# Kernel optimization log

Hardware: AMD Instinct MI355X
Metric: run time of the kernel (lower is better)

The kernel has to match this reference:

```python
import jax, jax.numpy as jnp
import numpy as np

B, S, E = 4, 2048, 1024
H, HD, R = 16, 64, 32  # heads, head_dim, rank


def setup_inputs() -> dict:
    key = jax.random.key(0)
    ks = jax.random.split(key, 9)
    sc = 0.02
    return {
        "hidden_states": jax.random.normal(ks[0], (B, S, E), jnp.float32),
        "q_weight": jax.random.normal(ks[1], (E, E), jnp.float32) * sc,
        "q_bias": jax.random.normal(ks[2], (E,), jnp.float32) * sc,
        "k_weight": jax.random.normal(ks[3], (E, E), jnp.float32) * sc,
        "k_bias": jax.random.normal(ks[4], (E,), jnp.float32) * sc,
        "low_rank_value_weight": jax.random.normal(ks[5], (E, H * R), jnp.float32) * sc,
        "low_rank_value_bias": jax.random.normal(ks[6], (H * R,), jnp.float32) * sc,
        "low_rank_output_weight": jax.random.normal(ks[7], (H * R, E), jnp.float32) * sc,
        "output_bias": jax.random.normal(ks[8], (E,), jnp.float32) * sc,
    }


def reference(hidden_states, q_weight, q_bias, k_weight, k_bias,
              low_rank_value_weight, low_rank_value_bias,
              low_rank_output_weight, output_bias):
    b, s, _ = hidden_states.shape
    q = hidden_states @ q_weight + q_bias                       # [B,S,E]
    k = hidden_states @ k_weight + k_bias                       # [B,S,E]
    v = hidden_states @ low_rank_value_weight + low_rank_value_bias  # [B,S,H*R]
    q = q.reshape(b, s, H, HD).transpose(0, 2, 1, 3)            # [B,H,S,HD]
    k = k.reshape(b, s, H, HD).transpose(0, 2, 1, 3)
    v = v.reshape(b, s, H, R).transpose(0, 2, 1, 3)             # [B,H,S,R]
    scores = jnp.einsum('bhqd,bhkd->bhqk', q, k) / jnp.sqrt(jnp.float32(HD))
    causal = jnp.tril(jnp.ones((s, s), dtype=bool))
    scores = jnp.where(causal, scores, jnp.finfo(scores.dtype).min)
    probs = jax.nn.softmax(scores, axis=-1)                     # [B,H,S,S]
    attn = jnp.einsum('bhqk,bhkr->bhqr', probs, v)              # [B,H,S,R]
    attn = attn.transpose(0, 2, 1, 3).reshape(b, s, H * R)      # [B,S,H*R]
    out = attn @ low_rank_output_weight + output_bias           # [B,S,E]
    return out
```

## Files before the change

kernel.cpp:

```cpp
#include <hip/hip_runtime.h>

typedef _Float16 f16;
typedef __attribute__((ext_vector_type(4))) float f4;
typedef __attribute__((ext_vector_type(4))) _Float16 h4;
typedef __attribute__((ext_vector_type(8))) _Float16 h8;
typedef __attribute__((ext_vector_type(4))) float f32x4;
typedef __attribute__((ext_vector_type(4))) unsigned int u4;

#define SWZ(row, colByte) (((row) << 7) + ((colByte) ^ (((row) & 7) << 4)))

__global__ __launch_bounds__(256) void cast_f16(
    const float* __restrict__ in, f16* __restrict__ out, int n4) {
  for (int i = blockIdx.x * 256 + threadIdx.x; i < n4; i += gridDim.x * 256) {
    const f4 v = ((const f4*)in)[i];
    h4 h;
    h.x = (f16)v.x; h.y = (f16)v.y; h.z = (f16)v.z; h.w = (f16)v.w;
    ((h4*)out)[i] = h;
  }
}

__global__ __launch_bounds__(256) void transpose_cast(
    const float* __restrict__ in, f16* __restrict__ out, int R, int C) {
  __shared__ float tile[32][33];
  const int t = threadIdx.x, tx = t & 31, ty = t >> 5;
  const int bc = blockIdx.x * 32, br = blockIdx.y * 32;
#pragma unroll
  for (int i = 0; i < 4; ++i)
    tile[ty + i * 8][tx] = in[(size_t)(br + ty + i * 8) * C + bc + tx];
  __syncthreads();
#pragma unroll
  for (int i = 0; i < 4; ++i)
    out[(size_t)(bc + ty + i * 8) * R + br + tx] = (f16)tile[tx][ty + i * 8];
}

__global__ __launch_bounds__(256) void hgemm_qkv(
    const f16* __restrict__ A, const f16* __restrict__ Bt,
    const float* __restrict__ qb, const float* __restrict__ kb,
    const float* __restrict__ vb,
    f16* __restrict__ qf, f16* __restrict__ kf, f16* __restrict__ vf) {
  __shared__ f16 As[128 * 40];
  __shared__ f16 Bs[128 * 40];
  const int K = 1024;
  const int id = blockIdx.x;
  const int swz = (id & 7) * 160 + (id >> 3);
  const int bnT = swz % 20;
  const int bm = (swz / 20) * 128;
  const int bn = bnT * 128;
  const int t = threadIdx.x;
  const int lane = t & 63, wave = t >> 6;
  const int wr = wave >> 1, wc = wave & 1;
  const int lrow = lane & 15, lk = lane >> 4;

  f32x4 acc[4][4];
#pragma unroll
  for (int i = 0; i < 4; ++i)
#pragma unroll
    for (int j = 0; j < 4; ++j) acc[i][j] = (f32x4)0.f;

  for (int kt = 0; kt < K; kt += 32) {
#pragma unroll
    for (int i = 0; i < 2; ++i) {
      const int ch = t + i * 256;
      const int row = ch >> 2, part = ch & 3;
      *(u4*)&As[row * 40 + part * 8] =
          *(const u4*)(A + (size_t)(bm + row) * K + kt + part * 8);
      *(u4*)&Bs[row * 40 + part * 8] =
          *(const u4*)(Bt + (size_t)(bn + row) * K + kt + part * 8);
    }
    __syncthreads();
    h8 af[4], bf[4];
#pragma unroll
    for (int f = 0; f < 4; ++f) {
      af[f] = *(const h8*)&As[(wr * 64 + f * 16 + lrow) * 40 + lk * 8];
      bf[f] = *(const h8*)&Bs[(wc * 64 + f * 16 + lrow) * 40 + lk * 8];
    }
#pragma unroll
    for (int i = 0; i < 4; ++i)
#pragma unroll
      for (int j = 0; j < 4; ++j)
        acc[i][j] = __builtin_amdgcn_mfma_f32_16x16x32_f16(af[i], bf[j], acc[i][j], 0, 0, 0);
    __syncthreads();
  }

  const float* bias;
  f16* outp;
  int nbase;
  if (bnT < 8) { bias = qb; outp = qf; nbase = 0; }
  else if (bnT < 16) { bias = kb; outp = kf; nbase = 1024; }
  else { bias = vb; outp = vf; nbase = 2048; }

#pragma unroll
  for (int fi = 0; fi < 4; ++fi) {
#pragma unroll
    for (int j = 0; j < 4; ++j) {
      const int grow = bm + wr * 64 + fi * 16 + lk * 4 + j;
      const int bb = grow >> 11, ss = grow & 2047;
#pragma unroll
      for (int fj = 0; fj < 4; ++fj) {
        const int gcol = bn + wc * 64 + fj * 16 + lrow;
        const int nl = gcol - nbase;
        const float g = acc[fi][fj][j] + bias[nl];
        if (bnT < 16) {
          outp[((size_t)(bb * 16 + (nl >> 6)) * 2048 + ss) * 64 + (nl & 63)] = (f16)g;
        } else {
          outp[((size_t)(bb * 16 + (nl >> 5)) * 2048 + ss) * 32 + (nl & 31)] = (f16)g;
        }
      }
    }
  }
}

__global__ __launch_bounds__(256) void hgemm_out(
    const f16* __restrict__ A, const f16* __restrict__ Bt,
    const float* __restrict__ bias, float* __restrict__ outp,
    const int N, const int K) {
  __shared__ f16 As[128 * 40];
  __shared__ f16 Bs[128 * 40];
  const int id = blockIdx.x;
  const int swz = (id & 7) * 64 + (id >> 3);
  const int bn = (swz & 7) * 128;
  const int bm = (swz >> 3) * 128;
  const int t = threadIdx.x;
  const int lane = t & 63, wave = t >> 6;
  const int wr = wave >> 1, wc = wave & 1;
  const int lrow = lane & 15, lk = lane >> 4;

  f32x4 acc[4][4];
#pragma unroll
  for (int i = 0; i < 4; ++i)
#pragma unroll
    for (int j = 0; j < 4; ++j) acc[i][j] = (f32x4)0.f;

  for (int kt = 0; kt < K; kt += 32) {
#pragma unroll
    for (int i = 0; i < 2; ++i) {
      const int ch = t + i * 256;
      const int row = ch >> 2, part = ch & 3;
      *(u4*)&As[row * 40 + part * 8] =
          *(const u4*)(A + (size_t)(bm + row) * K + kt + part * 8);
      *(u4*)&Bs[row * 40 + part * 8] =
          *(const u4*)(Bt + (size_t)(bn + row) * K + kt + part * 8);
    }
    __syncthreads();
    h8 af[4], bf[4];
#pragma unroll
    for (int f = 0; f < 4; ++f) {
      af[f] = *(const h8*)&As[(wr * 64 + f * 16 + lrow) * 40 + lk * 8];
      bf[f] = *(const h8*)&Bs[(wc * 64 + f * 16 + lrow) * 40 + lk * 8];
    }
#pragma unroll
    for (int i = 0; i < 4; ++i)
#pragma unroll
      for (int j = 0; j < 4; ++j)
        acc[i][j] = __builtin_amdgcn_mfma_f32_16x16x32_f16(af[i], bf[j], acc[i][j], 0, 0, 0);
    __syncthreads();
  }

#pragma unroll
  for (int fi = 0; fi < 4; ++fi) {
#pragma unroll
    for (int j = 0; j < 4; ++j) {
      const int grow = bm + wr * 64 + fi * 16 + lk * 4 + j;
#pragma unroll
      for (int fj = 0; fj < 4; ++fj) {
        const int gcol = bn + wc * 64 + fj * 16 + lrow;
        outp[(size_t)grow * N + gcol] = acc[fi][fj][j] + bias[gcol];
      }
    }
  }
}

__global__ __launch_bounds__(256) void attn_mfma(
    const f16* __restrict__ qf, const f16* __restrict__ kf,
    const f16* __restrict__ vf, f16* __restrict__ attf) {
  __shared__ f16 Ks[64 * 64];
  __shared__ f16 VsT[32 * 64];
  __shared__ f16 Ps[4 * 32 * 64];
  const int id = blockIdx.x;
  const int bh = id & 63;
  const int qblk = 15 - (id >> 6);
  const int qbase = qblk * 128;
  const int t = threadIdx.x;
  const int lane = t & 63, w = t >> 6;
  const int l15 = lane & 15, g = lane >> 4;
  const size_t kvbase = (size_t)bh * 2048;
  char* Pw = (char*)&Ps[w * 32 * 64];

  h8 qreg[2][2];
#pragma unroll
  for (int fj = 0; fj < 2; ++fj) {
    const int q = qbase + fj * 64 + w * 16 + l15;
#pragma unroll
    for (int ks = 0; ks < 2; ++ks) {
      h8 raw = *(const h8*)(qf + (kvbase + q) * 64 + ks * 32 + g * 8);
#pragma unroll
      for (int e = 0; e < 8; ++e) raw[e] = raw[e] * (f16)0.125f;
      qreg[fj][ks] = raw;
    }
  }

  f32x4 accO[2][2];
#pragma unroll
  for (int i = 0; i < 2; ++i)
#pragma unroll
    for (int j = 0; j < 2; ++j) accO[i][j] = (f32x4)0.f;
  float m2[2] = {-1.0e30f, -1.0e30f};
  float lsum[2] = {0.f, 0.f};

  const int ntiles = qblk * 2 + 2;
  for (int kt = 0; kt < ntiles; ++kt) {
    const int kbase = kt * 64;
    __syncthreads();
#pragma unroll
    for (int i = 0; i < 2; ++i) {
      const int idx = t + i * 256;
      const int row = idx >> 3, ch = idx & 7;
      *(u4*)((char*)Ks + SWZ(row, ch * 16)) =
          *(const u4*)(kf + (kvbase + kbase + row) * 64 + ch * 8);
    }
    {
      const int key = t >> 2, ch = t & 3;
      const u4 wv = *(const u4*)(vf + (kvbase + kbase + key) * 32 + ch * 8);
      const h8 hv = __builtin_bit_cast(h8, wv);
#pragma unroll
      for (int e = 0; e < 8; ++e) {
        const int row = ch * 8 + e;
        *(f16*)((char*)VsT + SWZ(row, key * 2)) = hv[e];
      }
    }
    __syncthreads();

    f32x4 accS[4][2];
#pragma unroll
    for (int i = 0; i < 4; ++i)
#pragma unroll
      for (int j = 0; j < 2; ++j) accS[i][j] = (f32x4)0.f;
#pragma unroll
    for (int ks = 0; ks < 2; ++ks) {
#pragma unroll
      for (int fim = 0; fim < 4; ++fim) {
        const h8 af = *(const h8*)((char*)Ks + SWZ(fim * 16 + l15, ks * 64 + g * 16));
#pragma unroll
        for (int fj = 0; fj < 2; ++fj)
          accS[fim][fj] = __builtin_amdgcn_mfma_f32_16x16x32_f16(af, qreg[fj][ks], accS[fim][fj], 0, 0, 0);
      }
    }

#pragma unroll
    for (int fj = 0; fj < 2; ++fj) {
      const int qg = qbase + fj * 64 + w * 16 + l15;
      const bool need_mask = (kbase + 63 > qbase + fj * 64 + w * 16);
      float sc[4][4];
      float mc = -1.0e30f;
#pragma unroll
      for (int fim = 0; fim < 4; ++fim)
#pragma unroll
        for (int j = 0; j < 4; ++j) {
          float v = accS[fim][fj][j];
          if (need_mask) {
            const int key = kbase + fim * 16 + g * 4 + j;
            v = (key <= qg) ? v : -1.0e30f;
          }
          sc[fim][j] = v;
          mc = fmaxf(mc, v);
        }
      mc = fmaxf(mc, __shfl_xor(mc, 16));
      mc = fmaxf(mc, __shfl_xor(mc, 32));
      if (!__all(mc <= m2[fj] + 1.5f)) {
        const float mnew = fmaxf(m2[fj], mc);
        const float corr = __expf(m2[fj] - mnew);
        m2[fj] = mnew;
        lsum[fj] *= corr;
#pragma unroll
        for (int j = 0; j < 4; ++j) {
          const float c = __shfl(corr, g * 4 + j);
          accO[fj][0][j] *= c;
          accO[fj][1][j] *= c;
        }
      }
      const float mloc = m2[fj];
      float ls = lsum[fj];
#pragma unroll
      for (int fim = 0; fim < 4; ++fim) {
        h4 hp;
#pragma unroll
        for (int j = 0; j < 4; ++j) {
          const float p = __expf(sc[fim][j] - mloc);
          ls += p;
          hp[j] = (f16)p;
        }
        *(h4*)(Pw + SWZ(fj * 16 + l15, fim * 32 + g * 8)) = hp;
      }
      lsum[fj] = ls;
    }

#pragma unroll
    for (int ks = 0; ks < 2; ++ks) {
      const h8 pa0 = *(const h8*)(Pw + SWZ(l15, ks * 64 + g * 16));
      const h8 pa1 = *(const h8*)(Pw + SWZ(16 + l15, ks * 64 + g * 16));
#pragma unroll
      for (int fr = 0; fr < 2; ++fr) {
        const h8 vb = *(const h8*)((char*)VsT + SWZ(fr * 16 + l15, ks * 64 + g * 16));
        accO[0][fr] = __builtin_amdgcn_mfma_f32_16x16x32_f16(pa0, vb, accO[0][fr], 0, 0, 0);
        accO[1][fr] = __builtin_amdgcn_mfma_f32_16x16x32_f16(pa1, vb, accO[1][fr], 0, 0, 0);
      }
    }
  }

  float inv[2];
#pragma unroll
  for (int fj = 0; fj < 2; ++fj) {
    float ls = lsum[fj];
    ls += __shfl_xor(ls, 16);
    ls += __shfl_xor(ls, 32);
    inv[fj] = 1.f / ls;
  }
  const int b = bh >> 4, h = bh & 15;
#pragma unroll
  for (int fo = 0; fo < 2; ++fo) {
#pragma unroll
    for (int j = 0; j < 4; ++j) {
      const float iv = __shfl(inv[fo], g * 4 + j);
      const int q = qbase + fo * 64 + w * 16 + g * 4 + j;
#pragma unroll
      for (int fr = 0; fr < 2; ++fr) {
        const int r = fr * 16 + l15;
        attf[((size_t)b * 2048 + q) * 512 + h * 32 + r] = (f16)(accO[fo][fr][j] * iv);
      }
    }
  }
}

extern "C" void kernel_launch(void* const* d_in, const int* in_sizes, int n_in,
                              void* d_out, int out_size, void* d_ws, size_t ws_size,
                              hipStream_t stream) {
  const float* hs = (const float*)d_in[0];
  const float* qw = (const float*)d_in[1];
  const float* qb = (const float*)d_in[2];
  const float* kw = (const float*)d_in[3];
  const float* kb = (const float*)d_in[4];
  const float* vw = (const float*)d_in[5];
  const float* vb = (const float*)d_in[6];
  const float* ow = (const float*)d_in[7];
  const float* ob = (const float*)d_in[8];
  float* out = (float*)d_out;
  char* ws = (char*)d_ws;

  f16* qf = (f16*)(ws);
  f16* kf = (f16*)(ws + ((size_t)16 << 20));
  f16* vf = (f16*)(ws + ((size_t)32 << 20));
  f16* attf = (f16*)(ws + ((size_t)40 << 20));
  f16* wqkv = (f16*)(ws + ((size_t)48 << 20));
  f16* owt = (f16*)(ws + ((size_t)54 << 20));
  f16* hsf = (f16*)(ws + ((size_t)56 << 20));

  cast_f16<<<2048, 256, 0, stream>>>(hs, hsf, 8192 * 1024 / 4);
  transpose_cast<<<dim3(32, 32), 256, 0, stream>>>(qw, wqkv, 1024, 1024);
  transpose_cast<<<dim3(32, 32), 256, 0, stream>>>(kw, wqkv + (size_t)1024 * 1024, 1024, 1024);
  transpose_cast<<<dim3(16, 32), 256, 0, stream>>>(vw, wqkv + (size_t)2048 * 1024, 1024, 512);
  transpose_cast<<<dim3(32, 16), 256, 0, stream>>>(ow, owt, 512, 1024);

  hgemm_qkv<<<dim3(1280), 256, 0, stream>>>(hsf, wqkv, qb, kb, vb, qf, kf, vf);
  attn_mfma<<<dim3(1024), 256, 0, stream>>>(qf, kf, vf, attf);
  hgemm_out<<<dim3(512), 256, 0, stream>>>(attf, owt, ob, out, 1024, 512);
}
```

Baseline: 176.9 us.

## Fuse casts into GEMM, merge transposes, pre-transpose V, MFMA row sums, exp2

Removes the separate hidden-state cast kernel by converting fp32 to fp16 inside the QKV GEMM's A-tile load, and merges the four weight transpose launches into one kernel. The QKV epilogue now writes V transposed so the attention kernel can load V tiles with vector stores instead of scattered per-element LDS writes. Softmax row sums are computed with an extra MFMA against a ones vector, exp is replaced with native exp2 plus fused scale, and the LDS swizzle is changed to reduce bank conflicts. The trade-offs are a doubled fp32 read of the A operand inside the GEMM loop, strided scalar stores for V in the epilogue, and a few extra MFMAs per tile.

```diff
diff --git a/kernel.cpp b/kernel.cpp
--- a/kernel.cpp
+++ b/kernel.cpp
@@ -7,23 +7,38 @@
 typedef __attribute__((ext_vector_type(4))) float f32x4;
 typedef __attribute__((ext_vector_type(4))) unsigned int u4;
 
-#define SWZ(row, colByte) (((row) << 7) + ((colByte) ^ (((row) & 7) << 4)))
-
-__global__ __launch_bounds__(256) void cast_f16(
-    const float* __restrict__ in, f16* __restrict__ out, int n4) {
-  for (int i = blockIdx.x * 256 + threadIdx.x; i < n4; i += gridDim.x * 256) {
-    const f4 v = ((const f4*)in)[i];
-    h4 h;
-    h.x = (f16)v.x; h.y = (f16)v.y; h.z = (f16)v.z; h.w = (f16)v.w;
-    ((h4*)out)[i] = h;
-  }
-}
-
-__global__ __launch_bounds__(256) void transpose_cast(
-    const float* __restrict__ in, f16* __restrict__ out, int R, int C) {
+extern "C" __device__ __attribute__((const)) float __ocml_native_exp2_f32(float);
+#define EXP2F __ocml_native_exp2_f32
+#define L2E 1.4426950408889634f
+
+#define SWZ(row, colByte) \
+  (((row) << 7) + ((colByte) ^ (((((row) ^ ((row) >> 3))) & 7) << 4)))
+
+__global__ __launch_bounds__(256) void transpose_all(
+    const float* __restrict__ qw, const float* __restrict__ kw,
+    const float* __restrict__ vw, const float* __restrict__ ow,
+    f16* __restrict__ wqkv, f16* __restrict__ owt) {
   __shared__ float tile[32][33];
+  int bid = blockIdx.x;
+  const float* in;
+  f16* out;
+  int R, C, bx, by;
+  if (bid < 1024) {
+    in = qw; out = wqkv; R = 1024; C = 1024; bx = bid & 31; by = bid >> 5;
+  } else if (bid < 2048) {
+    bid -= 1024;
+    in = kw; out = wqkv + (size_t)1024 * 1024; R = 1024; C = 1024;
+    bx = bid & 31; by = bid >> 5;
+  } else if (bid < 2560) {
+    bid -= 2048;
+    in = vw; out = wqkv + (size_t)2048 * 1024; R = 1024; C = 512;
+    bx = bid & 15; by = bid >> 4;
+  } else {
+    bid -= 2560;
+    in = ow; out = owt; R = 512; C = 1024; bx = bid & 31; by = bid >> 5;
+  }
   const int t = threadIdx.x, tx = t & 31, ty = t >> 5;
-  const int bc = blockIdx.x * 32, br = blockIdx.y * 32;
+  const int bc = bx * 32, br = by * 32;
 #pragma unroll
   for (int i = 0; i < 4; ++i)
     tile[ty + i * 8][tx] = in[(size_t)(br + ty + i * 8) * C + bc + tx];
@@ -34,10 +49,10 @@
 }
 
 __global__ __launch_bounds__(256) void hgemm_qkv(
-    const f16* __restrict__ A, const f16* __restrict__ Bt,
+    const float* __restrict__ A, const f16* __restrict__ Bt,
     const float* __restrict__ qb, const float* __restrict__ kb,
     const float* __restrict__ vb,
-    f16* __restrict__ qf, f16* __restrict__ kf, f16* __restrict__ vf) {
+    f16* __restrict__ qf, f16* __restrict__ kf, f16* __restrict__ vfT) {
   __shared__ f16 As[128 * 40];
   __shared__ f16 Bs[128 * 40];
   const int K = 1024;
@@ -62,8 +77,13 @@
     for (int i = 0; i < 2; ++i) {
       const int ch = t + i * 256;
       const int row = ch >> 2, part = ch & 3;
-      *(u4*)&As[row * 40 + part * 8] =
-          *(const u4*)(A + (size_t)(bm + row) * K + kt + part * 8);
+      const float* src = A + (size_t)(bm + row) * K + kt + part * 8;
+      const f4 v0 = *(const f4*)(src);
+      const f4 v1 = *(const f4*)(src + 4);
+      h8 hv;
+      hv[0] = (f16)v0.x; hv[1] = (f16)v0.y; hv[2] = (f16)v0.z; hv[3] = (f16)v0.w;
+      hv[4] = (f16)v1.x; hv[5] = (f16)v1.y; hv[6] = (f16)v1.z; hv[7] = (f16)v1.w;
+      *(h8*)&As[row * 40 + part * 8] = hv;
       *(u4*)&Bs[row * 40 + part * 8] =
           *(const u4*)(Bt + (size_t)(bn + row) * K + kt + part * 8);
     }
@@ -83,11 +103,10 @@
   }
 
   const float* bias;
-  f16* outp;
   int nbase;
-  if (bnT < 8) { bias = qb; outp = qf; nbase = 0; }
-  else if (bnT < 16) { bias = kb; outp = kf; nbase = 1024; }
-  else { bias = vb; outp = vf; nbase = 2048; }
+  if (bnT < 8) { bias = qb; nbase = 0; }
+  else if (bnT < 16) { bias = kb; nbase = 1024; }
+  else { bias = vb; nbase = 2048; }
 
 #pragma unroll
   for (int fi = 0; fi < 4; ++fi) {
@@ -100,10 +119,12 @@
         const int gcol = bn + wc * 64 + fj * 16 + lrow;
         const int nl = gcol - nbase;
         const float g = acc[fi][fj][j] + bias[nl];
-        if (bnT < 16) {
-          outp[((size_t)(bb * 16 + (nl >> 6)) * 2048 + ss) * 64 + (nl & 63)] = (f16)g;
+        if (bnT < 8) {
+          qf[((size_t)(bb * 16 + (nl >> 6)) * 2048 + ss) * 64 + (nl & 63)] = (f16)g;
+        } else if (bnT < 16) {
+          kf[((size_t)(bb * 16 + (nl >> 6)) * 2048 + ss) * 64 + (nl & 63)] = (f16)g;
         } else {
-          outp[((size_t)(bb * 16 + (nl >> 5)) * 2048 + ss) * 32 + (nl & 31)] = (f16)g;
+          vfT[((size_t)(bb * 16 + (nl >> 5)) * 32 + (nl & 31)) * 2048 + ss] = (f16)g;
         }
       }
     }
@@ -172,7 +193,7 @@
 
 __global__ __launch_bounds__(256) void attn_mfma(
     const f16* __restrict__ qf, const f16* __restrict__ kf,
-    const f16* __restrict__ vf, f16* __restrict__ attf) {
+    const f16* __restrict__ vfT, f16* __restrict__ attf) {
   __shared__ f16 Ks[64 * 64];
   __shared__ f16 VsT[32 * 64];
   __shared__ f16 Ps[4 * 32 * 64];
@@ -186,6 +207,10 @@
   const size_t kvbase = (size_t)bh * 2048;
   char* Pw = (char*)&Ps[w * 32 * 64];
 
+  h8 ones;
+#pragma unroll
+  for (int e = 0; e < 8; ++e) ones[e] = (f16)1.0f;
+
   h8 qreg[2][2];
 #pragma unroll
   for (int fj = 0; fj < 2; ++fj) {
@@ -200,12 +225,14 @@
   }
 
   f32x4 accO[2][2];
-#pragma unroll
-  for (int i = 0; i < 2; ++i)
+  f32x4 accL[2];
+#pragma unroll
+  for (int i = 0; i < 2; ++i) {
+    accL[i] = (f32x4)0.f;
 #pragma unroll
     for (int j = 0; j < 2; ++j) accO[i][j] = (f32x4)0.f;
+  }
   float m2[2] = {-1.0e30f, -1.0e30f};
-  float lsum[2] = {0.f, 0.f};
 
   const int ntiles = qblk * 2 + 2;
   for (int kt = 0; kt < ntiles; ++kt) {
@@ -219,14 +246,9 @@
           *(const u4*)(kf + (kvbase + kbase + row) * 64 + ch * 8);
     }
     {
-      const int key = t >> 2, ch = t & 3;
-      const u4 wv = *(const u4*)(vf + (kvbase + kbase + key) * 32 + ch * 8);
-      const h8 hv = __builtin_bit_cast(h8, wv);
-#pragma unroll
-      for (int e = 0; e < 8; ++e) {
-        const int row = ch * 8 + e;
-        *(f16*)((char*)VsT + SWZ(row, key * 2)) = hv[e];
-      }
+      const int row = t >> 3, ch = t & 7;
+      *(u4*)((char*)VsT + SWZ(row, ch * 16)) =
+          *(const u4*)(vfT + ((size_t)bh * 32 + row) * 2048 + kbase + ch * 8);
     }
     __syncthreads();
 
@@ -251,7 +273,6 @@
       const int qg = qbase + fj * 64 + w * 16 + l15;
       const bool need_mask = (kbase + 63 > qbase + fj * 64 + w * 16);
       float sc[4][4];
-      float mc = -1.0e30f;
 #pragma unroll
       for (int fim = 0; fim < 4; ++fim)
 #pragma unroll
@@ -262,36 +283,37 @@
             v = (key <= qg) ? v : -1.0e30f;
           }
           sc[fim][j] = v;
-          mc = fmaxf(mc, v);
         }
+      const float a0 = fmaxf(fmaxf(sc[0][0], sc[0][1]), sc[0][2]);
+      const float a1 = fmaxf(fmaxf(sc[0][3], sc[1][0]), sc[1][1]);
+      const float a2 = fmaxf(fmaxf(sc[1][2], sc[1][3]), sc[2][0]);
+      const float a3 = fmaxf(fmaxf(sc[2][1], sc[2][2]), sc[2][3]);
+      const float a4 = fmaxf(fmaxf(sc[3][0], sc[3][1]), sc[3][2]);
+      float mc = fmaxf(fmaxf(fmaxf(a0, a1), a2),
+                       fmaxf(fmaxf(a3, a4), sc[3][3]));
       mc = fmaxf(mc, __shfl_xor(mc, 16));
       mc = fmaxf(mc, __shfl_xor(mc, 32));
       if (!__all(mc <= m2[fj] + 1.5f)) {
         const float mnew = fmaxf(m2[fj], mc);
         const float corr = __expf(m2[fj] - mnew);
         m2[fj] = mnew;
-        lsum[fj] *= corr;
 #pragma unroll
         for (int j = 0; j < 4; ++j) {
           const float c = __shfl(corr, g * 4 + j);
           accO[fj][0][j] *= c;
           accO[fj][1][j] *= c;
+          accL[fj][j] *= c;
         }
       }
-      const float mloc = m2[fj];
-      float ls = lsum[fj];
+      const float nml = -m2[fj] * L2E;
 #pragma unroll
       for (int fim = 0; fim < 4; ++fim) {
         h4 hp;
 #pragma unroll
-        for (int j = 0; j < 4; ++j) {
-          const float p = __expf(sc[fim][j] - mloc);
-          ls += p;
-          hp[j] = (f16)p;
-        }
+        for (int j = 0; j < 4; ++j)
+          hp[j] = (f16)EXP2F(fmaf(sc[fim][j], L2E, nml));
         *(h4*)(Pw + SWZ(fj * 16 + l15, fim * 32 + g * 8)) = hp;
       }
-      lsum[fj] = ls;
     }
 
 #pragma unroll
@@ -304,23 +326,17 @@
         accO[0][fr] = __builtin_amdgcn_mfma_f32_16x16x32_f16(pa0, vb, accO[0][fr], 0, 0, 0);
         accO[1][fr] = __builtin_amdgcn_mfma_f32_16x16x32_f16(pa1, vb, accO[1][fr], 0, 0, 0);
       }
-    }
-  }
-
-  float inv[2];
-#pragma unroll
-  for (int fj = 0; fj < 2; ++fj) {
-    float ls = lsum[fj];
-    ls += __shfl_xor(ls, 16);
-    ls += __shfl_xor(ls, 32);
-    inv[fj] = 1.f / ls;
-  }
+      accL[0] = __builtin_amdgcn_mfma_f32_16x16x32_f16(pa0, ones, accL[0], 0, 0, 0);
+      accL[1] = __builtin_amdgcn_mfma_f32_16x16x32_f16(pa1, ones, accL[1], 0, 0, 0);
+    }
+  }
+
   const int b = bh >> 4, h = bh & 15;
 #pragma unroll
   for (int fo = 0; fo < 2; ++fo) {
 #pragma unroll
     for (int j = 0; j < 4; ++j) {
-      const float iv = __shfl(inv[fo], g * 4 + j);
+      const float iv = 1.f / accL[fo][j];
       const int q = qbase + fo * 64 + w * 16 + g * 4 + j;
 #pragma unroll
       for (int fr = 0; fr < 2; ++fr) {
@@ -348,19 +364,13 @@
 
   f16* qf = (f16*)(ws);
   f16* kf = (f16*)(ws + ((size_t)16 << 20));
-  f16* vf = (f16*)(ws + ((size_t)32 << 20));
+  f16* vfT = (f16*)(ws + ((size_t)32 << 20));
   f16* attf = (f16*)(ws + ((size_t)40 << 20));
   f16* wqkv = (f16*)(ws + ((size_t)48 << 20));
-  f16* owt = (f16*)(ws + ((size_t)54 << 20));
-  f16* hsf = (f16*)(ws + ((size_t)56 << 20));
-
-  cast_f16<<<2048, 256, 0, stream>>>(hs, hsf, 8192 * 1024 / 4);
-  transpose_cast<<<dim3(32, 32), 256, 0, stream>>>(qw, wqkv, 1024, 1024);
-  transpose_cast<<<dim3(32, 32), 256, 0, stream>>>(kw, wqkv + (size_t)1024 * 1024, 1024, 1024);
-  transpose_cast<<<dim3(16, 32), 256, 0, stream>>>(vw, wqkv + (size_t)2048 * 1024, 1024, 512);
-  transpose_cast<<<dim3(32, 16), 256, 0, stream>>>(ow, owt, 512, 1024);
-
-  hgemm_qkv<<<dim3(1280), 256, 0, stream>>>(hsf, wqkv, qb, kb, vb, qf, kf, vf);
-  attn_mfma<<<dim3(1024), 256, 0, stream>>>(qf, kf, vf, attf);
+  f16* owt = (f16*)(ws + ((size_t)53 << 20));
+
+  transpose_all<<<dim3(3072), 256, 0, stream>>>(qw, kw, vw, ow, wqkv, owt);
+  hgemm_qkv<<<dim3(1280), 256, 0, stream>>>(hs, wqkv, qb, kb, vb, qf, kf, vfT);
+  attn_mfma<<<dim3(1024), 256, 0, stream>>>(qf, kf, vfT, attf);
   hgemm_out<<<dim3(512), 256, 0, stream>>>(attf, owt, ob, out, 1024, 512);
 }
```

After: 179.3 us. Within noise of the previous version (+1.3%).
